# Kernel optimization log

Measured on AMD Instinct MI355X. Metric: run time of the kernel, lower is better.

## Reference

```python
import jax, jax.numpy as jnp
import numpy as np

N_SRC, N_DST, N_EDGES = 60000, 50000, 600000
IN_DIM, OUT_DIM = 256, 128


def setup_inputs() -> dict:
    key = jax.random.key(0)
    k1, k2, k3, k4, k5, k6 = jax.random.split(key, 6)
    features = jax.random.normal(k1, (N_SRC, IN_DIM), dtype=jnp.float32)
    t = jax.random.uniform(k2, (N_SRC,), dtype=jnp.float32)
    edge_src = jax.random.randint(k3, (N_EDGES,), 0, N_SRC, dtype=jnp.int32)
    edge_dst = jax.random.randint(k4, (N_EDGES,), 0, N_DST, dtype=jnp.int32)
    # learned params: xavier_normal with relu gain for fc, default for temporal_fc
    gain = float(np.sqrt(2.0))
    std_fc = gain * np.sqrt(2.0 / (IN_DIM + OUT_DIM))
    W_fc = jax.random.normal(k5, (OUT_DIM, IN_DIM), dtype=jnp.float32) * std_fc
    W_t = jax.random.normal(k6, (1, OUT_DIM), dtype=jnp.float32) * (1.0 / np.sqrt(OUT_DIM))
    return {"features": features, "t": t, "edge_src": edge_src,
            "edge_dst": edge_dst, "n_dst": N_DST, "W_fc": W_fc, "W_t": W_t}


def reference(features, t, edge_src, edge_dst, n_dst, W_fc, W_t):
    # z = fc(h), no bias
    z = features @ W_fc.T                      # [n_src, out_dim]
    s = (z @ W_t.T)[:, 0]                      # temporal_fc(z) -> [n_src]
    # edge attention: e = -|t_src - t_dst| (non-differentiable in original)
    e = jax.lax.stop_gradient(-jnp.abs(t[edge_src] - t[edge_dst]))  # [E]
    # mailbox logits: exp(temporal_fc(z_src) * e / 500)
    y = jnp.exp(s[edge_src] * e / 500.0)       # [E]
    # segment softmax over incoming edges of each dst node
    m = jax.ops.segment_max(y, edge_dst, num_segments=n_dst)
    m = jnp.where(jnp.isfinite(m), m, 0.0)     # empty mailboxes
    ex = jnp.exp(y - m[edge_dst])
    denom = jax.ops.segment_sum(ex, edge_dst, num_segments=n_dst)
    alpha = ex / denom[edge_dst]               # [E]
    # weighted neighbor sum
    h = jax.ops.segment_sum(alpha[:, None] * z[edge_src], edge_dst, num_segments=n_dst)
    # residual
    return z[:n_dst] + h
```

## Files before the change

### kernel.cpp

```cpp
#include <hip/hip_runtime.h>
#include <cstdint>

#define NBINS 1024
#define EPB   4096
#define MAXE  1536

typedef __attribute__((ext_vector_type(8))) _Float16 half8;
typedef __attribute__((ext_vector_type(4))) float floatx4;

__global__ __launch_bounds__(512, 4) void gemm_hist(
    const float* __restrict__ A, const float* __restrict__ W,
    const float* __restrict__ Wt, const int* __restrict__ edst,
    _Float16* __restrict__ z16, float* __restrict__ s,
    int* __restrict__ gcount, int M, int E, int NBH)
{
    __shared__ __align__(16) unsigned char smem[65536];

    if ((int)blockIdx.x < NBH) {
        int* h = (int*)smem;
        for (int i = threadIdx.x; i < NBINS; i += 512) h[i] = 0;
        __syncthreads();
        int base = blockIdx.x * EPB + threadIdx.x * 8;
        if (base + 8 <= E) {
            int4 d0 = *(const int4*)(edst + base);
            int4 d1 = *(const int4*)(edst + base + 4);
            atomicAdd(&h[d0.x >> 6], 1); atomicAdd(&h[d0.y >> 6], 1);
            atomicAdd(&h[d0.z >> 6], 1); atomicAdd(&h[d0.w >> 6], 1);
            atomicAdd(&h[d1.x >> 6], 1); atomicAdd(&h[d1.y >> 6], 1);
            atomicAdd(&h[d1.z >> 6], 1); atomicAdd(&h[d1.w >> 6], 1);
        } else {
            for (int i = 0; i < 8; ++i)
                if (base + i < E) atomicAdd(&h[edst[base + i] >> 6], 1);
        }
        __syncthreads();
        for (int i = threadIdx.x; i < NBINS; i += 512)
            gcount[(size_t)blockIdx.x * NBINS + i] = h[i];
        return;
    }

    half8* Wlds = (half8*)smem;
    const int tile = blockIdx.x - NBH;
    const int tid  = threadIdx.x;
    const int lane = tid & 63;
    const int w    = tid >> 6;
    const int m    = lane & 15;
    const int q    = lane >> 4;

#pragma unroll
    for (int it = 0; it < 8; ++it) {
        int pair = w * 8 + it;
        int nt = pair & 7, ks = pair >> 3;
        const float* src = W + (size_t)(nt * 16 + m) * 256 + ks * 32 + q * 8;
        float4 w0 = *(const float4*)src;
        float4 w1 = *(const float4*)(src + 4);
        half8 h;
        h[0] = (_Float16)w0.x; h[1] = (_Float16)w0.y;
        h[2] = (_Float16)w0.z; h[3] = (_Float16)w0.w;
        h[4] = (_Float16)w1.x; h[5] = (_Float16)w1.y;
        h[6] = (_Float16)w1.z; h[7] = (_Float16)w1.w;
        Wlds[pair * 64 + lane] = h;
    }

    const int row_base = tile * 128 + w * 16;
    const int arow = min(row_base + m, M - 1);
    const float* ap = A + (size_t)arow * 256 + q * 8;

    float4 abuf[8];
#pragma unroll
    for (int i = 0; i < 4; ++i) {
        abuf[2 * i]     = *(const float4*)(ap + i * 32);
        abuf[2 * i + 1] = *(const float4*)(ap + i * 32 + 4);
    }

    floatx4 acc[8];
#pragma unroll
    for (int nt = 0; nt < 8; ++nt) acc[nt] = (floatx4){0.f, 0.f, 0.f, 0.f};

    __syncthreads();

#pragma unroll
    for (int ks = 0; ks < 8; ++ks) {
        float4 a0 = abuf[(ks & 3) * 2];
        float4 a1 = abuf[(ks & 3) * 2 + 1];
        half8 af;
        af[0] = (_Float16)a0.x; af[1] = (_Float16)a0.y;
        af[2] = (_Float16)a0.z; af[3] = (_Float16)a0.w;
        af[4] = (_Float16)a1.x; af[5] = (_Float16)a1.y;
        af[6] = (_Float16)a1.z; af[7] = (_Float16)a1.w;

        if (ks < 4) {
            abuf[(ks & 3) * 2]     = *(const float4*)(ap + (ks + 4) * 32);
            abuf[(ks & 3) * 2 + 1] = *(const float4*)(ap + (ks + 4) * 32 + 4);
        }

#pragma unroll
        for (int nt = 0; nt < 8; ++nt) {
            half8 bf = Wlds[(ks * 8 + nt) * 64 + lane];
            acc[nt] = __builtin_amdgcn_mfma_f32_16x16x32_f16(
                af, bf, acc[nt], 0, 0, 0);
        }
    }

    float wt[8];
#pragma unroll
    for (int nt = 0; nt < 8; ++nt) wt[nt] = Wt[nt * 16 + m];

    float sp[4] = {0.f, 0.f, 0.f, 0.f};
#pragma unroll
    for (int nt = 0; nt < 8; ++nt)
#pragma unroll
        for (int reg = 0; reg < 4; ++reg)
            sp[reg] += acc[nt][reg] * wt[nt];

#pragma unroll
    for (int reg = 0; reg < 4; ++reg) {
        int row = row_base + q * 4 + reg;
        if (row < M) {
#pragma unroll
            for (int nt = 0; nt < 8; ++nt)
                z16[(size_t)row * 128 + nt * 16 + m] = (_Float16)acc[nt][reg];
        }
    }
#pragma unroll
    for (int off = 1; off <= 8; off <<= 1)
#pragma unroll
        for (int reg = 0; reg < 4; ++reg)
            sp[reg] += __shfl_xor(sp[reg], off, 64);
    if (m == 0) {
#pragma unroll
        for (int reg = 0; reg < 4; ++reg) {
            int row = row_base + q * 4 + reg;
            if (row < M) s[row] = sp[reg];
        }
    }
}

__global__ __launch_bounds__(256) void part_scan(
    int* __restrict__ gcount, int* __restrict__ binTot, int NB)
{
    int b = blockIdx.x * 256 + threadIdx.x;
    int run = 0;
    int blk = 0;
    for (; blk + 4 <= NB; blk += 4) {
        int v0 = gcount[(size_t)(blk + 0) * NBINS + b];
        int v1 = gcount[(size_t)(blk + 1) * NBINS + b];
        int v2 = gcount[(size_t)(blk + 2) * NBINS + b];
        int v3 = gcount[(size_t)(blk + 3) * NBINS + b];
        gcount[(size_t)(blk + 0) * NBINS + b] = run; run += v0;
        gcount[(size_t)(blk + 1) * NBINS + b] = run; run += v1;
        gcount[(size_t)(blk + 2) * NBINS + b] = run; run += v2;
        gcount[(size_t)(blk + 3) * NBINS + b] = run; run += v3;
    }
    for (; blk < NB; ++blk) {
        int v = gcount[(size_t)blk * NBINS + b];
        gcount[(size_t)blk * NBINS + b] = run; run += v;
    }
    binTot[b] = run;
}

__global__ __launch_bounds__(1024) void part_scanB(
    const int* __restrict__ binTot, int* __restrict__ binstart)
{
    __shared__ int wsum[16];
    int b = threadIdx.x;
    int lane = b & 63, wv = b >> 6;
    int v = binTot[b];
    int x = v;
#pragma unroll
    for (int off = 1; off < 64; off <<= 1) {
        int n = __shfl_up(x, off, 64);
        if (lane >= off) x += n;
    }
    if (lane == 63) wsum[wv] = x;
    __syncthreads();
    if (b < 64) {
        int t = (b < 16) ? wsum[b] : 0;
#pragma unroll
        for (int off = 1; off < 16; off <<= 1) {
            int n = __shfl_up(t, off, 64);
            if (lane >= off) t += n;
        }
        if (b < 16) wsum[b] = t;
    }
    __syncthreads();
    int base = (wv > 0) ? wsum[wv - 1] : 0;
    binstart[b] = base + x - v;
    if (b == NBINS - 1) binstart[NBINS] = base + x;
}

__global__ __launch_bounds__(512) void part_scatter(
    const int* __restrict__ esrc, const int* __restrict__ edst,
    const float* __restrict__ t, const float* __restrict__ s,
    const int* __restrict__ gcount, const int* __restrict__ binstart,
    int2* __restrict__ part, int E)
{
    __shared__ int hloc[NBINS];
    __shared__ int hbase[NBINS];
    for (int i = threadIdx.x; i < NBINS; i += 512) hloc[i] = 0;
    __syncthreads();

    int base = blockIdx.x * EPB + threadIdx.x * 8;
    int si[8], di[8], rk[8];
    int nv = 0;
    if (base < E) {
        nv = E - base; if (nv > 8) nv = 8;
        if (nv == 8) {
            int4 s0 = *(const int4*)(esrc + base);
            int4 s1 = *(const int4*)(esrc + base + 4);
            int4 d0 = *(const int4*)(edst + base);
            int4 d1 = *(const int4*)(edst + base + 4);
            si[0]=s0.x; si[1]=s0.y; si[2]=s0.z; si[3]=s0.w;
            si[4]=s1.x; si[5]=s1.y; si[6]=s1.z; si[7]=s1.w;
            di[0]=d0.x; di[1]=d0.y; di[2]=d0.z; di[3]=d0.w;
            di[4]=d1.x; di[5]=d1.y; di[6]=d1.z; di[7]=d1.w;
        } else {
            for (int i = 0; i < 8; ++i) {
                int e = min(base + i, E - 1);
                si[i] = esrc[e]; di[i] = edst[e];
            }
        }
#pragma unroll
        for (int i = 0; i < 8; ++i)
            if (i < nv) rk[i] = atomicAdd(&hloc[di[i] >> 6], 1);
    }

    for (int i = threadIdx.x; i < NBINS; i += 512)
        hbase[i] = binstart[i] + gcount[(size_t)blockIdx.x * NBINS + i];
    __syncthreads();

#pragma unroll
    for (int i = 0; i < 8; ++i) {
        if (i < nv) {
            float ee = -fabsf(t[si[i]] - t[di[i]]);
            float exv = __expf(__expf(s[si[i]] * ee * (1.0f / 500.0f)));
            part[hbase[di[i] >> 6] + rk[i]] =
                make_int2((si[i] & 0xffff) | ((di[i] & 63) << 16),
                          __float_as_int(exv));
        }
    }
}

__global__ __launch_bounds__(512, 4) void aggregate(
    const _Float16* __restrict__ z16, const int* __restrict__ binstart,
    const int2* __restrict__ part, float* __restrict__ out, int Nd)
{
    __shared__ int2 arr[MAXE];
    __shared__ int lcnt[64];
    __shared__ int loff[65];

    const int tid = threadIdx.x;
    const int b = blockIdx.x;
    const int s0 = binstart[b];
    int nE = binstart[b + 1] - s0;
    if (nE > MAXE) nE = MAXE;

    if (tid < 64) lcnt[tid] = 0;
    __syncthreads();

    int2 rec[3]; int rrk[3], rloc[3], nrec = 0;
    for (int i = tid; i < nE; i += 512) {
        int2 r = part[s0 + i];
        int loc = (r.x >> 16) & 63;
        rec[nrec] = r;
        rloc[nrec] = loc;
        rrk[nrec] = atomicAdd(&lcnt[loc], 1);
        ++nrec;
    }
    __syncthreads();
    if (tid < 64) {
        int v = lcnt[tid], x = v;
#pragma unroll
        for (int off = 1; off < 64; off <<= 1) {
            int n = __shfl_up(x, off, 64);
            if (tid >= off) x += n;
        }
        loff[tid + 1] = x;
        if (tid == 0) loff[0] = 0;
    }
    __syncthreads();
    for (int i = 0; i < nrec; ++i)
        arr[loff[rloc[i]] + rrk[i]] = rec[i];
    __syncthreads();

    const int lane = tid & 63;
    const int w = tid >> 6;
    const int g = lane >> 3;
    const int c = lane & 7;

    const int loc = w * 8 + g;
    const int jb = loff[loc], je = loff[loc + 1];

    float acc[16];
#pragma unroll
    for (int i = 0; i < 16; ++i) acc[i] = 0.f;
    float ds = 0.f;

    for (int j = jb; j < je; j += 4) {
        bool vB = j + 1 < je, vC = j + 2 < je, vD = j + 3 < je;
        int2 rA = arr[j];
        int2 rB = arr[vB ? j + 1 : 0];
        int2 rC = arr[vC ? j + 2 : 0];
        int2 rD = arr[vD ? j + 3 : 0];
        float xA = __int_as_float(rA.y);
        float xB = vB ? __int_as_float(rB.y) : 0.f;
        float xC = vC ? __int_as_float(rC.y) : 0.f;
        float xD = vD ? __int_as_float(rD.y) : 0.f;
        const half8* pA = (const half8*)(z16 + (size_t)(rA.x & 0xffff) * 128 + c * 16);
        const half8* pB = (const half8*)(z16 + (size_t)(rB.x & 0xffff) * 128 + c * 16);
        const half8* pC = (const half8*)(z16 + (size_t)(rC.x & 0xffff) * 128 + c * 16);
        const half8* pD = (const half8*)(z16 + (size_t)(rD.x & 0xffff) * 128 + c * 16);
        half8 alo = pA[0], ahi = pA[1];
        half8 blo = pB[0], bhi = pB[1];
        half8 clo = pC[0], chi = pC[1];
        half8 dlo = pD[0], dhi = pD[1];
        ds += (xA + xB) + (xC + xD);
#pragma unroll
        for (int i = 0; i < 8; ++i) {
            acc[i]     = fmaf(xA, (float)alo[i], acc[i]);
            acc[8 + i] = fmaf(xA, (float)ahi[i], acc[8 + i]);
            acc[i]     = fmaf(xB, (float)blo[i], acc[i]);
            acc[8 + i] = fmaf(xB, (float)bhi[i], acc[8 + i]);
            acc[i]     = fmaf(xC, (float)clo[i], acc[i]);
            acc[8 + i] = fmaf(xC, (float)chi[i], acc[8 + i]);
            acc[i]     = fmaf(xD, (float)dlo[i], acc[i]);
            acc[8 + i] = fmaf(xD, (float)dhi[i], acc[8 + i]);
        }
    }

    int d = b * 64 + loc;
    if (d < Nd) {
        bool has = je > jb;
        float inv = has ? 1.0f / ds : 0.0f;
        const half8* zr = (const half8*)(z16 + (size_t)d * 128 + c * 16);
        half8 r0 = zr[0], r1 = zr[1];
        float* op = out + (size_t)d * 128 + c * 16;
        *(float4*)(op + 0)  = make_float4(fmaf(acc[0],  inv, (float)r0[0]),
                                          fmaf(acc[1],  inv, (float)r0[1]),
                                          fmaf(acc[2],  inv, (float)r0[2]),
                                          fmaf(acc[3],  inv, (float)r0[3]));
        *(float4*)(op + 4)  = make_float4(fmaf(acc[4],  inv, (float)r0[4]),
                                          fmaf(acc[5],  inv, (float)r0[5]),
                                          fmaf(acc[6],  inv, (float)r0[6]),
                                          fmaf(acc[7],  inv, (float)r0[7]));
        *(float4*)(op + 8)  = make_float4(fmaf(acc[8],  inv, (float)r1[0]),
                                          fmaf(acc[9],  inv, (float)r1[1]),
                                          fmaf(acc[10], inv, (float)r1[2]),
                                          fmaf(acc[11], inv, (float)r1[3]));
        *(float4*)(op + 12) = make_float4(fmaf(acc[12], inv, (float)r1[4]),
                                          fmaf(acc[13], inv, (float)r1[5]),
                                          fmaf(acc[14], inv, (float)r1[6]),
                                          fmaf(acc[15], inv, (float)r1[7]));
    }
}

extern "C" void kernel_launch(void* const* d_in, const int* in_sizes, int n_in,
                              void* d_out, int out_size, void* d_ws, size_t ws_size,
                              hipStream_t stream)
{
    const float* features = (const float*)d_in[0];
    const float* t        = (const float*)d_in[1];
    const int*   esrc     = (const int*)d_in[2];
    const int*   edst     = (const int*)d_in[3];
    const float* Wfc      = (const float*)d_in[5];
    const float* Wt       = (const float*)d_in[6];
    float* out = (float*)d_out;

    const int M  = in_sizes[1];
    const int E  = in_sizes[2];
    const int OD = in_sizes[6];
    const int Nd = out_size / OD;

    const int NBH = (E + EPB - 1) / EPB;
    const int GB  = (M + 127) / 128;

    _Float16* z16      = (_Float16*)d_ws;
    float*    s        = (float*)(z16 + (size_t)M * 128);
    int*      gcount   = (int*)(s + M);
    int*      binTot   = gcount + (size_t)NBH * NBINS;
    int*      binstart = binTot + NBINS;
    int2*     part     = (int2*)(binstart + NBINS + 4);

    gemm_hist<<<NBH + GB, 512, 0, stream>>>(features, Wfc, Wt, edst,
                                            z16, s, gcount, M, E, NBH);
    part_scan<<<NBINS / 256, 256, 0, stream>>>(gcount, binTot, NBH);
    part_scanB<<<1, 1024, 0, stream>>>(binTot, binstart);
    part_scatter<<<NBH, 512, 0, stream>>>(esrc, edst, t, s, gcount, binstart,
                                          part, E);
    aggregate<<<(Nd + 63) / 64, 512, 0, stream>>>(z16, binstart, part, out, Nd);
}
```

Measured before the change: 199.4 us.

## Parallelize bin scan across wavefronts and restructure aggregate gather with 16-lane rows

part_scan now assigns one wavefront per bin and uses a shuffle-based prefix scan over block chunks, replacing a serial per-thread loop over all histogram blocks. The aggregate kernel drops to 256 threads, each 16-lane group handling one destination row per pass over four passes. Each lane accumulates 8 columns and issues eight independent 16-byte gathers through inline asm before a single wait. This aims to raise memory-level parallelism on the z16 gathers and cut the latency of the serial scan. In exchange it serializes four passes per block and relies on hand-placed waitcnt and sched_barrier.

New measurement: 174.4 us. -12.5%, faster.

```diff
diff --git a/kernel.cpp b/kernel.cpp
--- a/kernel.cpp
+++ b/kernel.cpp
@@ -7,6 +7,12 @@
 
 typedef __attribute__((ext_vector_type(8))) _Float16 half8;
 typedef __attribute__((ext_vector_type(4))) float floatx4;
+
+__device__ __forceinline__ half8 gload16(const void* p) {
+    half8 v;
+    asm volatile("global_load_dwordx4 %0, %1, off" : "=v"(v) : "v"(p));
+    return v;
+}
 
 __global__ __launch_bounds__(512, 4) void gemm_hist(
     const float* __restrict__ A, const float* __restrict__ W,
@@ -138,24 +144,24 @@
 __global__ __launch_bounds__(256) void part_scan(
     int* __restrict__ gcount, int* __restrict__ binTot, int NB)
 {
-    int b = blockIdx.x * 256 + threadIdx.x;
+    int b    = blockIdx.x * 4 + (threadIdx.x >> 6);
+    int lane = threadIdx.x & 63;
+    if (b >= NBINS) return;
+    int chunks = (NB + 63) >> 6;
     int run = 0;
-    int blk = 0;
-    for (; blk + 4 <= NB; blk += 4) {
-        int v0 = gcount[(size_t)(blk + 0) * NBINS + b];
-        int v1 = gcount[(size_t)(blk + 1) * NBINS + b];
-        int v2 = gcount[(size_t)(blk + 2) * NBINS + b];
-        int v3 = gcount[(size_t)(blk + 3) * NBINS + b];
-        gcount[(size_t)(blk + 0) * NBINS + b] = run; run += v0;
-        gcount[(size_t)(blk + 1) * NBINS + b] = run; run += v1;
-        gcount[(size_t)(blk + 2) * NBINS + b] = run; run += v2;
-        gcount[(size_t)(blk + 3) * NBINS + b] = run; run += v3;
-    }
-    for (; blk < NB; ++blk) {
-        int v = gcount[(size_t)blk * NBINS + b];
-        gcount[(size_t)blk * NBINS + b] = run; run += v;
-    }
-    binTot[b] = run;
+    for (int c = 0; c < chunks; ++c) {
+        int blk = c * 64 + lane;
+        int v = (blk < NB) ? gcount[(size_t)blk * NBINS + b] : 0;
+        int incl = v;
+#pragma unroll
+        for (int off = 1; off < 64; off <<= 1) {
+            int n = __shfl_up(incl, off, 64);
+            if (lane >= off) incl += n;
+        }
+        if (blk < NB) gcount[(size_t)blk * NBINS + b] = run + incl - v;
+        run += __shfl(incl, 63, 64);
+    }
+    if (lane == 0) binTot[b] = run;
 }
 
 __global__ __launch_bounds__(1024) void part_scanB(
@@ -240,7 +246,7 @@
     }
 }
 
-__global__ __launch_bounds__(512, 4) void aggregate(
+__global__ __launch_bounds__(256) void aggregate(
     const _Float16* __restrict__ z16, const int* __restrict__ binstart,
     const int2* __restrict__ part, float* __restrict__ out, int Nd)
 {
@@ -257,8 +263,8 @@
     if (tid < 64) lcnt[tid] = 0;
     __syncthreads();
 
-    int2 rec[3]; int rrk[3], rloc[3], nrec = 0;
-    for (int i = tid; i < nE; i += 512) {
+    int2 rec[6]; int rrk[6], rloc[6], nrec = 0;
+    for (int i = tid; i < nE; i += 256) {
         int2 r = part[s0 + i];
         int loc = (r.x >> 16) & 63;
         rec[nrec] = r;
@@ -282,74 +288,70 @@
         arr[loff[rloc[i]] + rrk[i]] = rec[i];
     __syncthreads();
 
-    const int lane = tid & 63;
-    const int w = tid >> 6;
-    const int g = lane >> 3;
-    const int c = lane & 7;
-
-    const int loc = w * 8 + g;
-    const int jb = loff[loc], je = loff[loc + 1];
-
-    float acc[16];
-#pragma unroll
-    for (int i = 0; i < 16; ++i) acc[i] = 0.f;
-    float ds = 0.f;
-
-    for (int j = jb; j < je; j += 4) {
-        bool vB = j + 1 < je, vC = j + 2 < je, vD = j + 3 < je;
-        int2 rA = arr[j];
-        int2 rB = arr[vB ? j + 1 : 0];
-        int2 rC = arr[vC ? j + 2 : 0];
-        int2 rD = arr[vD ? j + 3 : 0];
-        float xA = __int_as_float(rA.y);
-        float xB = vB ? __int_as_float(rB.y) : 0.f;
-        float xC = vC ? __int_as_float(rC.y) : 0.f;
-        float xD = vD ? __int_as_float(rD.y) : 0.f;
-        const half8* pA = (const half8*)(z16 + (size_t)(rA.x & 0xffff) * 128 + c * 16);
-        const half8* pB = (const half8*)(z16 + (size_t)(rB.x & 0xffff) * 128 + c * 16);
-        const half8* pC = (const half8*)(z16 + (size_t)(rC.x & 0xffff) * 128 + c * 16);
-        const half8* pD = (const half8*)(z16 + (size_t)(rD.x & 0xffff) * 128 + c * 16);
-        half8 alo = pA[0], ahi = pA[1];
-        half8 blo = pB[0], bhi = pB[1];
-        half8 clo = pC[0], chi = pC[1];
-        half8 dlo = pD[0], dhi = pD[1];
-        ds += (xA + xB) + (xC + xD);
-#pragma unroll
-        for (int i = 0; i < 8; ++i) {
-            acc[i]     = fmaf(xA, (float)alo[i], acc[i]);
-            acc[8 + i] = fmaf(xA, (float)ahi[i], acc[8 + i]);
-            acc[i]     = fmaf(xB, (float)blo[i], acc[i]);
-            acc[8 + i] = fmaf(xB, (float)bhi[i], acc[8 + i]);
-            acc[i]     = fmaf(xC, (float)clo[i], acc[i]);
-            acc[8 + i] = fmaf(xC, (float)chi[i], acc[8 + i]);
-            acc[i]     = fmaf(xD, (float)dlo[i], acc[i]);
-            acc[8 + i] = fmaf(xD, (float)dhi[i], acc[8 + i]);
-        }
-    }
-
-    int d = b * 64 + loc;
-    if (d < Nd) {
-        bool has = je > jb;
-        float inv = has ? 1.0f / ds : 0.0f;
-        const half8* zr = (const half8*)(z16 + (size_t)d * 128 + c * 16);
-        half8 r0 = zr[0], r1 = zr[1];
-        float* op = out + (size_t)d * 128 + c * 16;
-        *(float4*)(op + 0)  = make_float4(fmaf(acc[0],  inv, (float)r0[0]),
-                                          fmaf(acc[1],  inv, (float)r0[1]),
-                                          fmaf(acc[2],  inv, (float)r0[2]),
-                                          fmaf(acc[3],  inv, (float)r0[3]));
-        *(float4*)(op + 4)  = make_float4(fmaf(acc[4],  inv, (float)r0[4]),
-                                          fmaf(acc[5],  inv, (float)r0[5]),
-                                          fmaf(acc[6],  inv, (float)r0[6]),
-                                          fmaf(acc[7],  inv, (float)r0[7]));
-        *(float4*)(op + 8)  = make_float4(fmaf(acc[8],  inv, (float)r1[0]),
-                                          fmaf(acc[9],  inv, (float)r1[1]),
-                                          fmaf(acc[10], inv, (float)r1[2]),
-                                          fmaf(acc[11], inv, (float)r1[3]));
-        *(float4*)(op + 12) = make_float4(fmaf(acc[12], inv, (float)r1[4]),
-                                          fmaf(acc[13], inv, (float)r1[5]),
-                                          fmaf(acc[14], inv, (float)r1[6]),
-                                          fmaf(acc[15], inv, (float)r1[7]));
+    const int g = tid >> 4;
+    const int l = tid & 15;
+
+#pragma unroll 1
+    for (int pass = 0; pass < 4; ++pass) {
+        const int loc = pass * 16 + g;
+        const int jb = loff[loc], je = loff[loc + 1];
+
+        float acc[8];
+#pragma unroll
+        for (int i = 0; i < 8; ++i) acc[i] = 0.f;
+        float ds = 0.f;
+
+        for (int j = jb; j < je; j += 8) {
+            float x[8];
+            const void* p[8];
+#pragma unroll
+            for (int k = 0; k < 8; ++k) {
+                bool vk = (j + k) < je;
+                int jj = vk ? (j + k) : (je - 1);
+                int2 r = arr[jj];
+                x[k] = vk ? __int_as_float(r.y) : 0.f;
+                p[k] = (const void*)(z16 + (size_t)(r.x & 0xffff) * 128 + l * 8);
+            }
+            half8 v0 = gload16(p[0]);
+            half8 v1 = gload16(p[1]);
+            half8 v2 = gload16(p[2]);
+            half8 v3 = gload16(p[3]);
+            half8 v4 = gload16(p[4]);
+            half8 v5 = gload16(p[5]);
+            half8 v6 = gload16(p[6]);
+            half8 v7 = gload16(p[7]);
+            asm volatile("s_waitcnt vmcnt(0)" ::: "memory");
+            __builtin_amdgcn_sched_barrier(0);
+            ds += ((x[0] + x[1]) + (x[2] + x[3])) +
+                  ((x[4] + x[5]) + (x[6] + x[7]));
+#pragma unroll
+            for (int i = 0; i < 8; ++i) {
+                acc[i] = fmaf(x[0], (float)v0[i], acc[i]);
+                acc[i] = fmaf(x[1], (float)v1[i], acc[i]);
+                acc[i] = fmaf(x[2], (float)v2[i], acc[i]);
+                acc[i] = fmaf(x[3], (float)v3[i], acc[i]);
+                acc[i] = fmaf(x[4], (float)v4[i], acc[i]);
+                acc[i] = fmaf(x[5], (float)v5[i], acc[i]);
+                acc[i] = fmaf(x[6], (float)v6[i], acc[i]);
+                acc[i] = fmaf(x[7], (float)v7[i], acc[i]);
+            }
+        }
+
+        int d = b * 64 + loc;
+        if (d < Nd) {
+            float inv = (je > jb) ? 1.0f / ds : 0.0f;
+            const half8* zr = (const half8*)(z16 + (size_t)d * 128 + l * 8);
+            half8 r0 = *zr;
+            float* op = out + (size_t)d * 128 + l * 8;
+            *(float4*)(op + 0) = make_float4(fmaf(acc[0], inv, (float)r0[0]),
+                                             fmaf(acc[1], inv, (float)r0[1]),
+                                             fmaf(acc[2], inv, (float)r0[2]),
+                                             fmaf(acc[3], inv, (float)r0[3]));
+            *(float4*)(op + 4) = make_float4(fmaf(acc[4], inv, (float)r0[4]),
+                                             fmaf(acc[5], inv, (float)r0[5]),
+                                             fmaf(acc[6], inv, (float)r0[6]),
+                                             fmaf(acc[7], inv, (float)r0[7]));
+        }
     }
 }
 
@@ -382,9 +384,9 @@
 
     gemm_hist<<<NBH + GB, 512, 0, stream>>>(features, Wfc, Wt, edst,
                                             z16, s, gcount, M, E, NBH);
-    part_scan<<<NBINS / 256, 256, 0, stream>>>(gcount, binTot, NBH);
+    part_scan<<<NBINS / 4, 256, 0, stream>>>(gcount, binTot, NBH);
     part_scanB<<<1, 1024, 0, stream>>>(binTot, binstart);
     part_scatter<<<NBH, 512, 0, stream>>>(esrc, edst, t, s, gcount, binstart,
                                           part, E);
-    aggregate<<<(Nd + 63) / 64, 512, 0, stream>>>(z16, binstart, part, out, Nd);
-}
+    aggregate<<<(Nd + 63) / 64, 256, 0, stream>>>(z16, binstart, part, out, Nd);
+}
```
